# Performance work log

Hardware: AMD Instinct MI355X
Metric: run time of the kernel (lower is better)

Reference implementation:

```python
import jax, jax.numpy as jnp
import numpy as np
import math

B, L, H, E = 4, 2048, 8, 64


def setup_inputs() -> dict:
    key = jax.random.key(0)
    kq, kk, kv, ks = jax.random.split(key, 4)
    return {
        "queries": jax.random.normal(kq, (B, L, H, E), dtype=jnp.float32),
        "keys": jax.random.normal(kk, (B, L, H, E), dtype=jnp.float32),
        "values": jax.random.normal(kv, (B, L, H, E), dtype=jnp.float32),
        "sigma": jax.random.normal(ks, (B, L, H), dtype=jnp.float32),
    }


def reference(queries, keys, values, sigma):
    Bq, Lq, Hq, Eq = queries.shape
    scale = 1.0 / math.sqrt(Eq)
    # QK^T: [B, H, L, S]
    scores = jnp.einsum("blhe,bshe->bhls", queries, keys)
    # triangular causal mask (mask_flag=True, attn_mask=None)
    causal = jnp.triu(jnp.ones((Lq, Lq), dtype=bool), k=1)
    scores = jnp.where(causal[None, None], -jnp.inf, scores)
    attn = scale * scores
    series = jax.nn.softmax(attn, axis=-1)  # dropout p=0.0 -> identity
    # sigma: [B, L, H] -> [B, H, L]
    sig = jnp.transpose(sigma, (0, 2, 1))
    sig = jax.nn.sigmoid(sig * 5.0) + 1e-5
    sig = jnp.power(3.0, sig) - 1.0
    sig = jnp.broadcast_to(sig[..., None], (Bq, Hq, Lq, Lq))  # [B,H,L,L]
    # |i - j| distances
    idx = jnp.arange(Lq, dtype=jnp.float32)
    dist = jnp.abs(idx[:, None] - idx[None, :])  # [L, L]
    prior = (1.0 / (math.sqrt(2.0 * math.pi) * sig)) * jnp.exp(
        -(dist[None, None] ** 2) / (2.0 * sig ** 2)
    )
    V = jnp.einsum("bhls,bshd->blhd", series, values)
    return V, series, prior, sig
```

## Files before the change

### kernel.cpp

```cpp
#include <hip/hip_runtime.h>
#include <math.h>

#define BB 4
#define LL 2048
#define HH 8
#define EE 64
#define TM 128
#define TN 64
#define SH 72

typedef _Float16 half4v __attribute__((ext_vector_type(4)));
typedef _Float16 half8v __attribute__((ext_vector_type(8)));
typedef float floatx4 __attribute__((ext_vector_type(4)));

static constexpr float SCALE = 0.125f;
static constexpr float LN3 = 1.0986122886681098f;
static constexpr float INV_SQRT_2PI = 0.3989422804014327f;
static constexpr size_t NMAT = (size_t)BB * HH * LL * LL;
static constexpr size_t SERIES_BASE = (size_t)BB * LL * HH * EE;
static constexpr size_t PRIOR_BASE = SERIES_BASE + NMAT;
static constexpr size_t SIG_BASE = PRIOR_BASE + NMAT;

__global__ __launch_bounds__(512, 2)
void anomaly_attn(const float* __restrict__ qg,
                  const float* __restrict__ kg,
                  const float* __restrict__ vg,
                  const float* __restrict__ sgg,
                  float* __restrict__ out) {
  __shared__ __attribute__((aligned(16))) _Float16 Qh[TM * SH];
  __shared__ __attribute__((aligned(16))) _Float16 Kh[TN * SH];
  __shared__ __attribute__((aligned(16))) _Float16 Vt[EE * SH];
  __shared__ __attribute__((aligned(16))) _Float16 Ph[TM * SH];
  __shared__ float s_sigv[TM], s_pinv[TM], s_c2[TM];

  const int t = threadIdx.x;
  const int lane = t & 63;
  const int w = t >> 6;
  const int quad = lane >> 4;
  const int l15 = lane & 15;
  const int bh = blockIdx.y;
  const int b = bh >> 3, h = bh & 7;
  const float4* q4 = (const float4*)qg;
  const float4* k4 = (const float4*)kg;
  const float4* v4 = (const float4*)vg;

  for (int half = 0; half < 2; ++half) {
    const int rt = half ? (15 - (int)blockIdx.x) : (int)blockIdx.x;
    const int i0 = rt * TM;
    const int nt = 2 * rt + 2;
    __syncthreads();

#pragma unroll
    for (int it = 0; it < 4; ++it) {
      int idx = t + 512 * it;
      int r = idx >> 4, c = idx & 15;
      float4 qv = q4[(((size_t)b * LL + i0 + r) * HH + h) * 16 + c];
      half4v hq = {(_Float16)qv.x, (_Float16)qv.y, (_Float16)qv.z, (_Float16)qv.w};
      *(half4v*)&Qh[r * SH + c * 4] = hq;
    }
    if (t < TM) {
      float sg = sgg[((size_t)b * LL + (i0 + t)) * HH + h];
      float sd = 1.0f / (1.0f + __expf(-5.0f * sg)) + 1e-5f;
      float sv = expm1f(sd * LN3);
      s_sigv[t] = sv;
      s_pinv[t] = INV_SQRT_2PI / sv;
      s_c2[t] = 0.5f / (sv * sv);
    }

    float lsum[4] = {0.f, 0.f, 0.f, 0.f};
    for (int jt = 0; jt < nt; ++jt) {
      const int j0 = jt * TN;
      __syncthreads();
#pragma unroll
      for (int it = 0; it < 2; ++it) {
        int idx = t + 512 * it;
        int r = idx >> 4, c = idx & 15;
        float4 kv = k4[(((size_t)b * LL + j0 + r) * HH + h) * 16 + c];
        half4v hk = {(_Float16)kv.x, (_Float16)kv.y, (_Float16)kv.z, (_Float16)kv.w};
        *(half4v*)&Kh[r * SH + c * 4] = hk;
      }
      __syncthreads();
      floatx4 acc[4] = {{0.f, 0.f, 0.f, 0.f}, {0.f, 0.f, 0.f, 0.f},
                        {0.f, 0.f, 0.f, 0.f}, {0.f, 0.f, 0.f, 0.f}};
#pragma unroll
      for (int ks = 0; ks < 2; ++ks) {
        half8v a = *(half8v*)&Qh[(w * 16 + l15) * SH + ks * 32 + quad * 8];
#pragma unroll
        for (int f = 0; f < 4; ++f) {
          half8v bf = *(half8v*)&Kh[(f * 16 + l15) * SH + ks * 32 + quad * 8];
          acc[f] = __builtin_amdgcn_mfma_f32_16x16x32_f16(a, bf, acc[f], 0, 0, 0);
        }
      }
#pragma unroll
      for (int f = 0; f < 4; ++f) {
        int j = j0 + f * 16 + l15;
#pragma unroll
        for (int r = 0; r < 4; ++r) {
          int i = i0 + w * 16 + quad * 4 + r;
          lsum[r] += (j <= i) ? __expf(acc[f][r] * SCALE) : 0.f;
        }
      }
    }
#pragma unroll
    for (int r = 0; r < 4; ++r) {
      lsum[r] += __shfl_xor(lsum[r], 1);
      lsum[r] += __shfl_xor(lsum[r], 2);
      lsum[r] += __shfl_xor(lsum[r], 4);
      lsum[r] += __shfl_xor(lsum[r], 8);
    }
    float linv[4];
#pragma unroll
    for (int r = 0; r < 4; ++r) linv[r] = 1.0f / lsum[r];

    floatx4 Oacc[4] = {{0.f, 0.f, 0.f, 0.f}, {0.f, 0.f, 0.f, 0.f},
                       {0.f, 0.f, 0.f, 0.f}, {0.f, 0.f, 0.f, 0.f}};
    for (int jt = 0; jt < nt; ++jt) {
      const int j0 = jt * TN;
      __syncthreads();
      if (t < 256) {
        const int tx = t & 15, ty = t >> 4;
        float4 vv[4];
#pragma unroll
        for (int rr = 0; rr < 4; ++rr)
          vv[rr] = v4[(((size_t)b * LL + j0 + ty * 4 + rr) * HH + h) * 16 + tx];
#pragma unroll
        for (int c = 0; c < 4; ++c) {
          float e0 = c == 0 ? vv[0].x : c == 1 ? vv[0].y : c == 2 ? vv[0].z : vv[0].w;
          float e1 = c == 0 ? vv[1].x : c == 1 ? vv[1].y : c == 2 ? vv[1].z : vv[1].w;
          float e2 = c == 0 ? vv[2].x : c == 1 ? vv[2].y : c == 2 ? vv[2].z : vv[2].w;
          float e3 = c == 0 ? vv[3].x : c == 1 ? vv[3].y : c == 2 ? vv[3].z : vv[3].w;
          half4v hv = {(_Float16)e0, (_Float16)e1, (_Float16)e2, (_Float16)e3};
          *(half4v*)&Vt[(tx * 4 + c) * SH + ty * 4] = hv;
        }
      } else {
        const int tk = t - 256;
#pragma unroll
        for (int it = 0; it < 4; ++it) {
          int idx = tk + 256 * it;
          int r = idx >> 4, c = idx & 15;
          float4 kv = k4[(((size_t)b * LL + j0 + r) * HH + h) * 16 + c];
          half4v hk = {(_Float16)kv.x, (_Float16)kv.y, (_Float16)kv.z, (_Float16)kv.w};
          *(half4v*)&Kh[r * SH + c * 4] = hk;
        }
      }
      __syncthreads();
      floatx4 acc[4] = {{0.f, 0.f, 0.f, 0.f}, {0.f, 0.f, 0.f, 0.f},
                        {0.f, 0.f, 0.f, 0.f}, {0.f, 0.f, 0.f, 0.f}};
#pragma unroll
      for (int ks = 0; ks < 2; ++ks) {
        half8v a = *(half8v*)&Qh[(w * 16 + l15) * SH + ks * 32 + quad * 8];
#pragma unroll
        for (int f = 0; f < 4; ++f) {
          half8v bf = *(half8v*)&Kh[(f * 16 + l15) * SH + ks * 32 + quad * 8];
          acc[f] = __builtin_amdgcn_mfma_f32_16x16x32_f16(a, bf, acc[f], 0, 0, 0);
        }
      }
#pragma unroll
      for (int f = 0; f < 4; ++f) {
        int j = j0 + f * 16 + l15;
#pragma unroll
        for (int r = 0; r < 4; ++r) {
          int i = i0 + w * 16 + quad * 4 + r;
          float p = (j <= i) ? __expf(acc[f][r] * SCALE) * linv[r] : 0.f;
          Ph[(w * 16 + quad * 4 + r) * SH + f * 16 + l15] = (_Float16)p;
        }
      }
#pragma unroll
      for (int rnd = 0; rnd < 2; ++rnd) {
        int row = w * 16 + rnd * 8 + (lane >> 3);
        int c8 = lane & 7;
        half8v p = *(half8v*)&Ph[row * SH + c8 * 8];
        floatx4 lo = {(float)p[0], (float)p[1], (float)p[2], (float)p[3]};
        floatx4 hi = {(float)p[4], (float)p[5], (float)p[6], (float)p[7]};
        size_t off = SERIES_BASE + ((size_t)bh * LL + i0 + row) * LL + j0 + c8 * 8;
        *(floatx4*)&out[off] = lo;
        *(floatx4*)&out[off + 4] = hi;
      }
      __syncthreads();
#pragma unroll
      for (int ks = 0; ks < 2; ++ks) {
        half8v a = *(half8v*)&Ph[(w * 16 + l15) * SH + ks * 32 + quad * 8];
#pragma unroll
        for (int f = 0; f < 4; ++f) {
          half8v bv = *(half8v*)&Vt[(f * 16 + l15) * SH + ks * 32 + quad * 8];
          Oacc[f] = __builtin_amdgcn_mfma_f32_16x16x32_f16(a, bv, Oacc[f], 0, 0, 0);
        }
      }
    }
#pragma unroll
    for (int f = 0; f < 4; ++f) {
#pragma unroll
      for (int r = 0; r < 4; ++r) {
        int i = i0 + w * 16 + quad * 4 + r;
        out[(((size_t)b * LL + i) * HH + h) * EE + f * 16 + l15] = Oacc[f][r];
      }
    }
    for (int idx = t; idx < TM * 512; idx += 512) {
      int rr = idx >> 9, jq = idx & 511;
      float iv = s_pinv[rr], c2 = s_c2[rr], sv = s_sigv[rr];
      float fi = (float)(i0 + rr);
      float d0 = fi - (float)(jq * 4);
      float d1 = d0 - 1.0f, d2 = d0 - 2.0f, d3 = d0 - 3.0f;
      floatx4 pr;
      pr.x = iv * __expf(-d0 * d0 * c2);
      pr.y = iv * __expf(-d1 * d1 * c2);
      pr.z = iv * __expf(-d2 * d2 * c2);
      pr.w = iv * __expf(-d3 * d3 * c2);
      size_t off = ((size_t)bh * LL + (i0 + rr)) * LL + jq * 4;
      *(floatx4*)&out[PRIOR_BASE + off] = pr;
      floatx4 sg4 = {sv, sv, sv, sv};
      *(floatx4*)&out[SIG_BASE + off] = sg4;
    }
    {
      int jz = nt * TN;
      int nz4 = (LL - jz) >> 2;
      if (nz4 > 0) {
        const floatx4 z = {0.f, 0.f, 0.f, 0.f};
        for (int rr = 0; rr < TM; ++rr) {
          float* rowp = &out[SERIES_BASE + ((size_t)bh * LL + (i0 + rr)) * LL + jz];
          for (int c = t; c < nz4; c += 512) {
            *(floatx4*)&rowp[c * 4] = z;
          }
        }
      }
    }
  }
}

extern "C" void kernel_launch(void* const* d_in, const int* in_sizes, int n_in,
                              void* d_out, int out_size, void* d_ws, size_t ws_size,
                              hipStream_t stream) {
  const float* q = (const float*)d_in[0];
  const float* k = (const float*)d_in[1];
  const float* v = (const float*)d_in[2];
  const float* sg = (const float*)d_in[3];
  float* out = (float*)d_out;
  dim3 grid(16 / 2, BB * HH);
  anomaly_attn<<<grid, 512, 0, stream>>>(q, k, v, sg, out);
}
```

Before: 1.750 ms.

## Halve row tile, double-buffer K/V with register prefetch, use 256-thread blocks

Reduces the query row tile from 128 to 64 and the block from 512 to 256 threads, which doubles the grid to 512 blocks. K and V tiles now live in two LDS buffers: the next tile is prefetched into registers while the current one is used in MFMAs, then written to the spare buffer behind a single lgkmcnt-wait barrier. This removes one of the two barriers per tile and the barrier between the P write and the PV MFMA, aiming to hide global load latency and spread the large series/prior/sigma writes over more CUs. The cost is more register pressure from the prefetch and more repeated K/V reads, since each block now covers fewer rows.

```diff
diff --git a/kernel.cpp b/kernel.cpp
--- a/kernel.cpp
+++ b/kernel.cpp
@@ -5,7 +5,7 @@
 #define LL 2048
 #define HH 8
 #define EE 64
-#define TM 128
+#define TM 64
 #define TN 64
 #define SH 72
 
@@ -21,15 +21,21 @@
 static constexpr size_t PRIOR_BASE = SERIES_BASE + NMAT;
 static constexpr size_t SIG_BASE = PRIOR_BASE + NMAT;
 
-__global__ __launch_bounds__(512, 2)
+__device__ __forceinline__ void barrier_release() {
+  asm volatile("s_waitcnt lgkmcnt(0)" ::: "memory");
+  __builtin_amdgcn_s_barrier();
+  __builtin_amdgcn_sched_barrier(0);
+}
+
+__global__ __launch_bounds__(256, 2)
 void anomaly_attn(const float* __restrict__ qg,
                   const float* __restrict__ kg,
                   const float* __restrict__ vg,
                   const float* __restrict__ sgg,
                   float* __restrict__ out) {
   __shared__ __attribute__((aligned(16))) _Float16 Qh[TM * SH];
-  __shared__ __attribute__((aligned(16))) _Float16 Kh[TN * SH];
-  __shared__ __attribute__((aligned(16))) _Float16 Vt[EE * SH];
+  __shared__ __attribute__((aligned(16))) _Float16 Kh[2][TN * SH];
+  __shared__ __attribute__((aligned(16))) _Float16 Vt[2][EE * SH];
   __shared__ __attribute__((aligned(16))) _Float16 Ph[TM * SH];
   __shared__ float s_sigv[TM], s_pinv[TM], s_c2[TM];
 
@@ -44,15 +50,50 @@
   const float4* k4 = (const float4*)kg;
   const float4* v4 = (const float4*)vg;
 
+  const int kr_r0 = t >> 4, kr_c = t & 15;
+  const int vtx = t & 15, vty = t >> 4;
+
+  auto loadK = [&](int j0, float4* kr) {
+#pragma unroll
+    for (int it = 0; it < 4; ++it)
+      kr[it] = k4[(((size_t)b * LL + j0 + kr_r0 + 16 * it) * HH + h) * 16 + kr_c];
+  };
+  auto writeK = [&](int bufi, const float4* kr) {
+#pragma unroll
+    for (int it = 0; it < 4; ++it) {
+      half4v hk = {(_Float16)kr[it].x, (_Float16)kr[it].y,
+                   (_Float16)kr[it].z, (_Float16)kr[it].w};
+      *(half4v*)&Kh[bufi][(kr_r0 + 16 * it) * SH + kr_c * 4] = hk;
+    }
+  };
+  auto loadV = [&](int j0, float4* vr) {
+#pragma unroll
+    for (int rr = 0; rr < 4; ++rr)
+      vr[rr] = v4[(((size_t)b * LL + j0 + vty * 4 + rr) * HH + h) * 16 + vtx];
+  };
+  auto writeV = [&](int bufi, const float4* vr) {
+#pragma unroll
+    for (int c = 0; c < 4; ++c) {
+      float e0 = c == 0 ? vr[0].x : c == 1 ? vr[0].y : c == 2 ? vr[0].z : vr[0].w;
+      float e1 = c == 0 ? vr[1].x : c == 1 ? vr[1].y : c == 2 ? vr[1].z : vr[1].w;
+      float e2 = c == 0 ? vr[2].x : c == 1 ? vr[2].y : c == 2 ? vr[2].z : vr[2].w;
+      float e3 = c == 0 ? vr[3].x : c == 1 ? vr[3].y : c == 2 ? vr[3].z : vr[3].w;
+      half4v hv = {(_Float16)e0, (_Float16)e1, (_Float16)e2, (_Float16)e3};
+      *(half4v*)&Vt[bufi][(vtx * 4 + c) * SH + vty * 4] = hv;
+    }
+  };
+
   for (int half = 0; half < 2; ++half) {
-    const int rt = half ? (15 - (int)blockIdx.x) : (int)blockIdx.x;
+    const int rt = half ? (31 - (int)blockIdx.x) : (int)blockIdx.x;
     const int i0 = rt * TM;
-    const int nt = 2 * rt + 2;
+    const int nt = rt + 1;
     __syncthreads();
 
+    float4 kr[4], vr[4];
+    loadK(0, kr);
 #pragma unroll
     for (int it = 0; it < 4; ++it) {
-      int idx = t + 512 * it;
+      int idx = t + 256 * it;
       int r = idx >> 4, c = idx & 15;
       float4 qv = q4[(((size_t)b * LL + i0 + r) * HH + h) * 16 + c];
       half4v hq = {(_Float16)qv.x, (_Float16)qv.y, (_Float16)qv.z, (_Float16)qv.w};
@@ -66,20 +107,14 @@
       s_pinv[t] = INV_SQRT_2PI / sv;
       s_c2[t] = 0.5f / (sv * sv);
     }
+    writeK(0, kr);
+    barrier_release();
 
     float lsum[4] = {0.f, 0.f, 0.f, 0.f};
+    int cur = 0;
     for (int jt = 0; jt < nt; ++jt) {
-      const int j0 = jt * TN;
-      __syncthreads();
-#pragma unroll
-      for (int it = 0; it < 2; ++it) {
-        int idx = t + 512 * it;
-        int r = idx >> 4, c = idx & 15;
-        float4 kv = k4[(((size_t)b * LL + j0 + r) * HH + h) * 16 + c];
-        half4v hk = {(_Float16)kv.x, (_Float16)kv.y, (_Float16)kv.z, (_Float16)kv.w};
-        *(half4v*)&Kh[r * SH + c * 4] = hk;
-      }
-      __syncthreads();
+      const bool more = (jt + 1 < nt);
+      if (more) loadK((jt + 1) * TN, kr);
       floatx4 acc[4] = {{0.f, 0.f, 0.f, 0.f}, {0.f, 0.f, 0.f, 0.f},
                         {0.f, 0.f, 0.f, 0.f}, {0.f, 0.f, 0.f, 0.f}};
 #pragma unroll
@@ -87,10 +122,11 @@
         half8v a = *(half8v*)&Qh[(w * 16 + l15) * SH + ks * 32 + quad * 8];
 #pragma unroll
         for (int f = 0; f < 4; ++f) {
-          half8v bf = *(half8v*)&Kh[(f * 16 + l15) * SH + ks * 32 + quad * 8];
+          half8v bf = *(half8v*)&Kh[cur][(f * 16 + l15) * SH + ks * 32 + quad * 8];
           acc[f] = __builtin_amdgcn_mfma_f32_16x16x32_f16(a, bf, acc[f], 0, 0, 0);
         }
       }
+      const int j0 = jt * TN;
 #pragma unroll
       for (int f = 0; f < 4; ++f) {
         int j = j0 + f * 16 + l15;
@@ -99,6 +135,11 @@
           int i = i0 + w * 16 + quad * 4 + r;
           lsum[r] += (j <= i) ? __expf(acc[f][r] * SCALE) : 0.f;
         }
+      }
+      if (more) {
+        writeK(cur ^ 1, kr);
+        barrier_release();
+        cur ^= 1;
       }
     }
 #pragma unroll
@@ -114,36 +155,20 @@
 
     floatx4 Oacc[4] = {{0.f, 0.f, 0.f, 0.f}, {0.f, 0.f, 0.f, 0.f},
                        {0.f, 0.f, 0.f, 0.f}, {0.f, 0.f, 0.f, 0.f}};
+    loadK(0, kr);
+    loadV(0, vr);
+    __syncthreads();
+    writeK(0, kr);
+    writeV(0, vr);
+    barrier_release();
+    cur = 0;
     for (int jt = 0; jt < nt; ++jt) {
+      const bool more = (jt + 1 < nt);
       const int j0 = jt * TN;
-      __syncthreads();
-      if (t < 256) {
-        const int tx = t & 15, ty = t >> 4;
-        float4 vv[4];
-#pragma unroll
-        for (int rr = 0; rr < 4; ++rr)
-          vv[rr] = v4[(((size_t)b * LL + j0 + ty * 4 + rr) * HH + h) * 16 + tx];
-#pragma unroll
-        for (int c = 0; c < 4; ++c) {
-          float e0 = c == 0 ? vv[0].x : c == 1 ? vv[0].y : c == 2 ? vv[0].z : vv[0].w;
-          float e1 = c == 0 ? vv[1].x : c == 1 ? vv[1].y : c == 2 ? vv[1].z : vv[1].w;
-          float e2 = c == 0 ? vv[2].x : c == 1 ? vv[2].y : c == 2 ? vv[2].z : vv[2].w;
-          float e3 = c == 0 ? vv[3].x : c == 1 ? vv[3].y : c == 2 ? vv[3].z : vv[3].w;
-          half4v hv = {(_Float16)e0, (_Float16)e1, (_Float16)e2, (_Float16)e3};
-          *(half4v*)&Vt[(tx * 4 + c) * SH + ty * 4] = hv;
-        }
-      } else {
-        const int tk = t - 256;
-#pragma unroll
-        for (int it = 0; it < 4; ++it) {
-          int idx = tk + 256 * it;
-          int r = idx >> 4, c = idx & 15;
-          float4 kv = k4[(((size_t)b * LL + j0 + r) * HH + h) * 16 + c];
-          half4v hk = {(_Float16)kv.x, (_Float16)kv.y, (_Float16)kv.z, (_Float16)kv.w};
-          *(half4v*)&Kh[r * SH + c * 4] = hk;
-        }
-      }
-      __syncthreads();
+      if (more) {
+        loadK((jt + 1) * TN, kr);
+        loadV((jt + 1) * TN, vr);
+      }
       floatx4 acc[4] = {{0.f, 0.f, 0.f, 0.f}, {0.f, 0.f, 0.f, 0.f},
                         {0.f, 0.f, 0.f, 0.f}, {0.f, 0.f, 0.f, 0.f}};
 #pragma unroll
@@ -151,7 +176,7 @@
         half8v a = *(half8v*)&Qh[(w * 16 + l15) * SH + ks * 32 + quad * 8];
 #pragma unroll
         for (int f = 0; f < 4; ++f) {
-          half8v bf = *(half8v*)&Kh[(f * 16 + l15) * SH + ks * 32 + quad * 8];
+          half8v bf = *(half8v*)&Kh[cur][(f * 16 + l15) * SH + ks * 32 + quad * 8];
           acc[f] = __builtin_amdgcn_mfma_f32_16x16x32_f16(a, bf, acc[f], 0, 0, 0);
         }
       }
@@ -176,15 +201,20 @@
         *(floatx4*)&out[off] = lo;
         *(floatx4*)&out[off + 4] = hi;
       }
-      __syncthreads();
 #pragma unroll
       for (int ks = 0; ks < 2; ++ks) {
         half8v a = *(half8v*)&Ph[(w * 16 + l15) * SH + ks * 32 + quad * 8];
 #pragma unroll
         for (int f = 0; f < 4; ++f) {
-          half8v bv = *(half8v*)&Vt[(f * 16 + l15) * SH + ks * 32 + quad * 8];
+          half8v bv = *(half8v*)&Vt[cur][(f * 16 + l15) * SH + ks * 32 + quad * 8];
           Oacc[f] = __builtin_amdgcn_mfma_f32_16x16x32_f16(a, bv, Oacc[f], 0, 0, 0);
         }
+      }
+      if (more) {
+        writeK(cur ^ 1, kr);
+        writeV(cur ^ 1, vr);
+        barrier_release();
+        cur ^= 1;
       }
     }
 #pragma unroll
@@ -195,7 +225,7 @@
         out[(((size_t)b * LL + i) * HH + h) * EE + f * 16 + l15] = Oacc[f][r];
       }
     }
-    for (int idx = t; idx < TM * 512; idx += 512) {
+    for (int idx = t; idx < TM * 512; idx += 256) {
       int rr = idx >> 9, jq = idx & 511;
       float iv = s_pinv[rr], c2 = s_c2[rr], sv = s_sigv[rr];
       float fi = (float)(i0 + rr);
@@ -218,7 +248,7 @@
         const floatx4 z = {0.f, 0.f, 0.f, 0.f};
         for (int rr = 0; rr < TM; ++rr) {
           float* rowp = &out[SERIES_BASE + ((size_t)bh * LL + (i0 + rr)) * LL + jz];
-          for (int c = t; c < nz4; c += 512) {
+          for (int c = t; c < nz4; c += 256) {
             *(floatx4*)&rowp[c * 4] = z;
           }
         }
@@ -235,6 +265,6 @@
   const float* v = (const float*)d_in[2];
   const float* sg = (const float*)d_in[3];
   float* out = (float*)d_out;
-  dim3 grid(16 / 2, BB * HH);
-  anomaly_attn<<<grid, 512, 0, stream>>>(q, k, v, sg, out);
+  dim3 grid(LL / TM / 2, BB * HH);
+  anomaly_attn<<<grid, 256, 0, stream>>>(q, k, v, sg, out);
 }
```

New measurement: 1.690 ms. 1.04x faster.
